# Performance work log

Hardware: AMD Instinct MI355X
Metric: run time of the kernel (lower is better)

The kernel has to match this reference:

```python
import jax, jax.numpy as jnp
import numpy as np

B, L, C, H, DK = 2, 2048, 256, 8, 32  # batch, seq, feaSize, multiNum, dk


def setup_inputs() -> dict:
    key = jax.random.key(0)
    ks = jax.random.split(key, 11)
    w = lambda k, shape: jax.random.normal(k, shape, dtype=jnp.float32) * 0.02
    return {
        'qx': jax.random.normal(ks[0], (B, L, C), dtype=jnp.float32),
        'kx': jax.random.normal(ks[1], (B, L, C), dtype=jnp.float32),
        'vx': jax.random.normal(ks[2], (B, L, C), dtype=jnp.float32),
        'WQ': w(ks[3], (C, H * DK)), 'bQ': w(ks[4], (H * DK,)),
        'WK': w(ks[5], (C, H * DK)), 'bK': w(ks[6], (H * DK,)),
        'WV': w(ks[7], (C, H * DK)), 'bV': w(ks[8], (H * DK,)),
        'WO': w(ks[9], (H * DK, C)), 'bO': w(ks[10], (C,)),
    }


def reference(qx, kx, vx, WQ, bQ, WK, bK, WV, bV, WO, bO):
    b, l, c = qx.shape
    # projections -> (B, H, L, DK)
    q = (qx @ WQ + bQ).reshape(b, l, H, DK).transpose(0, 2, 1, 3)
    k = (kx @ WK + bK).reshape(b, l, H, DK).transpose(0, 2, 1, 3)
    v = (vx @ WV + bV).reshape(b, l, H, DK).transpose(0, 2, 1, 3)

    g = jnp.array([0, l - 1])  # global rows / cols
    scores = jnp.zeros((b, H, l, l), dtype=q.dtype)
    # global rows: q[0], q[L-1] attend to everything
    scores = scores.at[:, :, g, :].set(jnp.einsum('bhgd,bhld->bhgl', q[:, :, g, :], k))
    # global cols: everything attends to k[0], k[L-1]
    scores = scores.at[:, :, :, g].set(jnp.einsum('bhld,bhgd->bhlg', q, k[:, :, g, :]))
    # sliding window: super-diag, sub-diag, main diag (dot products along DK)
    i = jnp.arange(l - 1)
    scores = scores.at[:, :, i, i + 1].set(jnp.sum(q[:, :, :-1] * k[:, :, 1:], axis=-1))
    scores = scores.at[:, :, i + 1, i].set(jnp.sum(q[:, :, 1:] * k[:, :, :-1], axis=-1))
    d = jnp.arange(l)
    scores = scores.at[:, :, d, d].set(jnp.sum(q * k, axis=-1))
    # NOTE: the torch random-block write `scores[:,:,r,:][:,:,:,r] = ...` writes
    # into a copy (chained advanced indexing) and is therefore a no-op; we
    # faithfully omit it. Unfilled positions keep score 0 (not -inf), as in torch.
    scores = scores / np.float32(np.sqrt(DK))
    alpha = jax.nn.softmax(scores, axis=3)
    z = jnp.einsum('bhlm,bhmd->bhld', alpha, v)
    z = z.transpose(0, 2, 1, 3).reshape(b, l, H * DK)
    return z @ WO + bO
```

## Files before the change

### kernel.cpp

```cpp
#include <hip/hip_runtime.h>
#include <hip/hip_bf16.h>

#define B_   2
#define L_   2048
#define C_   256
#define H_   8
#define DK_  32
#define HD_  256
#define RSQRT_DK 0.17677669529663687f

typedef __attribute__((ext_vector_type(8))) short bf16x8;
typedef __attribute__((ext_vector_type(4))) float f32x4;
typedef __attribute__((ext_vector_type(4))) unsigned int u32x4;

__device__ __forceinline__ unsigned short f2bf(float x) {
    unsigned int u = __float_as_uint(x);
    u += 0x7fffu + ((u >> 16) & 1u);
    return (unsigned short)(u >> 16);
}
__device__ __forceinline__ float bf2f(unsigned short h) {
    return __uint_as_float((unsigned int)h << 16);
}

__device__ __forceinline__ uint2 split2(float x0, float x1) {
    __hip_bfloat162 h2 = __float22bfloat162_rn(make_float2(x0, x1));
    unsigned hu; __builtin_memcpy(&hu, &h2, 4);
    const float e0 = __uint_as_float(hu << 16);
    const float e1 = __uint_as_float(hu & 0xffff0000u);
    __hip_bfloat162 l2 = __float22bfloat162_rn(make_float2(x0 - e0, x1 - e1));
    unsigned lu; __builtin_memcpy(&lu, &l2, 4);
    return make_uint2(hu, lu);
}
__device__ __forceinline__ bf16x8 as_bf16x8(u32x4 v) {
    bf16x8 r; __builtin_memcpy(&r, &v, 16); return r;
}

#define WT_IDX(n, k) (((n) << 8) + (((((k) >> 3) ^ ((n) & 7))) << 3) + ((k) & 7))

__device__ __forceinline__ void stage_wT(
    const float* __restrict__ W, int n0, int tid,
    short* __restrict__ WTh, short* __restrict__ WTl)
{
    const int n  = tid & 63;
    const int kc = tid >> 6;
    #pragma unroll
    for (int c8 = 0; c8 < 8; ++c8) {
        const int k0 = kc * 64 + c8 * 8;
        u32x4 hv, lv;
        #pragma unroll
        for (int e = 0; e < 4; ++e) {
            const float x0 = W[(size_t)(k0 + 2 * e)     * HD_ + n0 + n];
            const float x1 = W[(size_t)(k0 + 2 * e + 1) * HD_ + n0 + n];
            const uint2 hl = split2(x0, x1);
            hv[e] = hl.x; lv[e] = hl.y;
        }
        const int o = (n << 8) + ((((k0 >> 3) ^ (n & 7))) << 3);
        *reinterpret_cast<u32x4*>(&WTh[o]) = hv;
        *reinterpret_cast<u32x4*>(&WTl[o]) = lv;
    }
}

__global__ __launch_bounds__(256) void gemm_qkv_fused(
    const float* __restrict__ qx, const float* __restrict__ kx, const float* __restrict__ vx,
    const float* __restrict__ WQ, const float* __restrict__ bQ,
    const float* __restrict__ WK, const float* __restrict__ bK,
    const float* __restrict__ WV, const float* __restrict__ bV,
    float* __restrict__ q, float* __restrict__ k, float* __restrict__ v,
    float* __restrict__ part)
{
    const int bx = blockIdx.x;
    const int yy = blockIdx.y;
    const int proj = yy >> 2, nt = yy & 3;
    const float* A    = proj == 0 ? qx : (proj == 1 ? kx : vx);
    const float* W    = proj == 0 ? WQ : (proj == 1 ? WK : WV);
    const float* bias = proj == 0 ? bQ : (proj == 1 ? bK : bV);
    float* out        = proj == 0 ? q  : (proj == 1 ? k  : v);
    const int n0 = nt * 64;

    __shared__ short WTh[64 * 256];
    __shared__ short WTl[64 * 256];
    __shared__ float red[4][4][16];

    const int tid = threadIdx.x;
    stage_wT(W, n0, tid, WTh, WTl);
    __syncthreads();

    const int w  = tid >> 6;
    const int l  = tid & 63;
    const int lm = l & 15, lk8 = (l >> 4) * 8, cr = (l >> 4) * 4;
    const int R  = bx * 128 + w * 32;

    f32x4 acc[2][4];
    #pragma unroll
    for (int mf = 0; mf < 2; ++mf)
        #pragma unroll
        for (int nf = 0; nf < 4; ++nf)
            acc[mf][nf] = (f32x4){0.f, 0.f, 0.f, 0.f};

    float4 Ab[2][4];
    #define LOAD_A(buf, ks)                                                          \
    {                                                                                \
        const float* p0 = &A[(size_t)(R + lm) * C_ + (ks) * 32 + lk8];               \
        const float* p1 = &A[(size_t)(R + 16 + lm) * C_ + (ks) * 32 + lk8];          \
        Ab[buf][0] = *reinterpret_cast<const float4*>(p0);                           \
        Ab[buf][1] = *reinterpret_cast<const float4*>(p0 + 4);                       \
        Ab[buf][2] = *reinterpret_cast<const float4*>(p1);                           \
        Ab[buf][3] = *reinterpret_cast<const float4*>(p1 + 4);                       \
    }
    LOAD_A(0, 0)
    LOAD_A(1, 1)

    #pragma unroll
    for (int ks = 0; ks < 8; ++ks) {
        const int cur = ks & 1;
        bf16x8 ah[2], al[2];
        #pragma unroll
        for (int mf = 0; mf < 2; ++mf) {
            float4 v0 = Ab[cur][mf * 2], v1 = Ab[cur][mf * 2 + 1];
            u32x4 hq, lq;
            {
                const uint2 r0 = split2(v0.x, v0.y);
                const uint2 r1 = split2(v0.z, v0.w);
                const uint2 r2 = split2(v1.x, v1.y);
                const uint2 r3 = split2(v1.z, v1.w);
                hq[0] = r0.x; lq[0] = r0.y;
                hq[1] = r1.x; lq[1] = r1.y;
                hq[2] = r2.x; lq[2] = r2.y;
                hq[3] = r3.x; lq[3] = r3.y;
            }
            ah[mf] = as_bf16x8(hq);
            al[mf] = as_bf16x8(lq);
        }
        if (ks < 6) LOAD_A(cur, ks + 2)
        bf16x8 Bh[4], Bl[4];
        #pragma unroll
        for (int nf = 0; nf < 4; ++nf) {
            const int o = WT_IDX(nf * 16 + lm, ks * 32 + lk8);
            Bh[nf] = *reinterpret_cast<const bf16x8*>(&WTh[o]);
            Bl[nf] = *reinterpret_cast<const bf16x8*>(&WTl[o]);
        }
        #pragma unroll
        for (int mf = 0; mf < 2; ++mf)
            #pragma unroll
            for (int nf = 0; nf < 4; ++nf) {
                acc[mf][nf] = __builtin_amdgcn_mfma_f32_16x16x32_bf16(ah[mf], Bh[nf], acc[mf][nf], 0, 0, 0);
                acc[mf][nf] = __builtin_amdgcn_mfma_f32_16x16x32_bf16(ah[mf], Bl[nf], acc[mf][nf], 0, 0, 0);
                acc[mf][nf] = __builtin_amdgcn_mfma_f32_16x16x32_bf16(al[mf], Bh[nf], acc[mf][nf], 0, 0, 0);
            }
    }
    #undef LOAD_A

    #pragma unroll
    for (int mf = 0; mf < 2; ++mf)
        #pragma unroll
        for (int nf = 0; nf < 4; ++nf) {
            const int col = n0 + nf * 16 + lm;
            const int h = col >> 5, d = col & 31;
            const float bb = bias[col];
            #pragma unroll
            for (int r = 0; r < 4; ++r) {
                const int m = R + mf * 16 + cr + r;
                const int b = m >> 11, lrow = m & (L_ - 1);
                out[((size_t)(b * H_ + h) * L_ + lrow) * DK_ + d] = acc[mf][nf][r] + bb;
            }
        }

    if (proj == 2) {
        float sl[4];
        #pragma unroll
        for (int nf = 0; nf < 4; ++nf) {
            float s = 0.f;
            #pragma unroll
            for (int mf = 0; mf < 2; ++mf)
                #pragma unroll
                for (int r = 0; r < 4; ++r) s += acc[mf][nf][r];
            s += __shfl_xor(s, 16);
            s += __shfl_xor(s, 32);
            sl[nf] = s;
        }
        if (l < 16) {
            #pragma unroll
            for (int nf = 0; nf < 4; ++nf) red[w][nf][l] = sl[nf];
        }
        __syncthreads();
        if (tid < 64) {
            const int nf = tid >> 4, lmm = tid & 15;
            float tot = red[0][nf][lmm] + red[1][nf][lmm] + red[2][nf][lmm] + red[3][nf][lmm];
            const int col = n0 + nf * 16 + lmm;
            tot += 128.f * bias[col];
            const int h = col >> 5, d = col & 31;
            const int bh = (bx >> 4) * H_ + h;
            part[((size_t)bh * 32 + d) * 16 + (bx & 15)] = tot;
        }
    }
}

#define NSLOT 264
#define VOFF  132

__global__ __launch_bounds__(128) void attn_main(
    const float* __restrict__ q, const float* __restrict__ k,
    const float* __restrict__ v, const float* __restrict__ part,
    float* __restrict__ pm, float* __restrict__ pZ, float* __restrict__ pzv,
    unsigned short* __restrict__ zh, unsigned short* __restrict__ zl)
{
    __shared__ float Sf[NSLOT * 32 + 32];
    float* vs_sh = &Sf[NSLOT * 32];

    #define LDS_F4(slot, u2) (*reinterpret_cast<const float4*>(&Sf[((slot) << 5) + (((u2) ^ ((slot) & 7)) << 2)]))

    const int blk = blockIdx.x;
    const int t = threadIdx.x;

    if (blk < 256) {
        const int bh = blk >> 4, c = blk & 15;
        const int base = c * 128;
        const float* qb = q + (size_t)bh * L_ * DK_;
        const float* kb = k + (size_t)bh * L_ * DK_;
        const float* vb = v + (size_t)bh * L_ * DK_;

        for (int u = t; u < 1056; u += 128) {
            const int slot = u >> 3, quad = u & 7;
            const int row = (slot < 130) ? min(base + slot, L_ - 1)
                                         : ((slot == 130) ? 0 : L_ - 1);
            const size_t go = (size_t)row * DK_ + quad * 4;
            float4 kw = *reinterpret_cast<const float4*>(&kb[go]);
            float4 vw = *reinterpret_cast<const float4*>(&vb[go]);
            const int so = ((quad ^ (slot & 7)) << 2);
            float* dk = &Sf[(slot << 5) + so];
            float* dv = &Sf[((slot + VOFF) << 5) + (((quad ^ ((slot + VOFF) & 7))) << 2)];
            dk[0] = kw.x; dk[1] = kw.y; dk[2] = kw.z; dk[3] = kw.w;
            dv[0] = vw.x; dv[1] = vw.y; dv[2] = vw.z; dv[3] = vw.w;
        }
        if (t < 32) {
            const float4* pp = reinterpret_cast<const float4*>(&part[((size_t)bh * 32 + t) * 16]);
            float4 pa = pp[0], pb = pp[1], pc = pp[2], pd = pp[3];
            vs_sh[t] = pa.x + pa.y + pa.z + pa.w + pb.x + pb.y + pb.z + pb.w
                     + pc.x + pc.y + pc.z + pc.w + pd.x + pd.y + pd.z + pd.w;
        }
        __syncthreads();

        const int i = base + 1 + t;
        if (i <= L_ - 2) {
            float qr[32];
            {
                const float4* qp = reinterpret_cast<const float4*>(&qb[(size_t)i * DK_]);
                #pragma unroll
                for (int u2 = 0; u2 < 8; ++u2) {
                    float4 x = qp[u2];
                    qr[u2 * 4 + 0] = x.x; qr[u2 * 4 + 1] = x.y;
                    qr[u2 * 4 + 2] = x.z; qr[u2 * 4 + 3] = x.w;
                }
            }
            const int ks_[5] = {130, t, t + 1, t + 2, 131};
            float sv[5];
            #pragma unroll
            for (int jj = 0; jj < 5; ++jj) {
                const int s = ks_[jj];
                float p = 0.f;
                #pragma unroll
                for (int u2 = 0; u2 < 8; ++u2) {
                    float4 kv = LDS_F4(s, u2);
                    p += qr[u2 * 4 + 0] * kv.x + qr[u2 * 4 + 1] * kv.y
                       + qr[u2 * 4 + 2] * kv.z + qr[u2 * 4 + 3] * kv.w;
                }
                sv[jj] = p * RSQRT_DK;
            }
            const bool v1 = (i != 1), v3 = (i != L_ - 2);
            float m = fmaxf(0.f, sv[0]);
            m = fmaxf(m, sv[2]); m = fmaxf(m, sv[4]);
            if (v1) m = fmaxf(m, sv[1]);
            if (v3) m = fmaxf(m, sv[3]);
            float e[5];
            e[0] = __expf(sv[0] - m);
            e[1] = v1 ? __expf(sv[1] - m) : 0.f;
            e[2] = __expf(sv[2] - m);
            e[3] = v3 ? __expf(sv[3] - m) : 0.f;
            e[4] = __expf(sv[4] - m);
            const int ns = 3 + (int)v1 + (int)v3;
            const float e0 = __expf(-m);
            const float Z = e[0] + e[1] + e[2] + e[3] + e[4] + (float)(L_ - ns) * e0;
            const float rZ = 1.f / Z;
            const float f1 = v1 ? 1.f : 0.f, f3 = v3 ? 1.f : 0.f;

            u32x4 zhq[4], zlq[4];
            #pragma unroll
            for (int u2 = 0; u2 < 8; ++u2) {
                float4 x0 = LDS_F4(VOFF + 130,   u2);
                float4 x1 = LDS_F4(VOFF + t,     u2);
                float4 x2 = LDS_F4(VOFF + t + 1, u2);
                float4 x3 = LDS_F4(VOFF + t + 2, u2);
                float4 x4 = LDS_F4(VOFF + 131,   u2);
                float a0[4] = {x0.x, x0.y, x0.z, x0.w};
                float a1[4] = {x1.x, x1.y, x1.z, x1.w};
                float a2[4] = {x2.x, x2.y, x2.z, x2.w};
                float a3[4] = {x3.x, x3.y, x3.z, x3.w};
                float a4[4] = {x4.x, x4.y, x4.z, x4.w};
                float zd4[4];
                #pragma unroll
                for (int e2 = 0; e2 < 4; ++e2) {
                    const int d = u2 * 4 + e2;
                    const float num = e[0] * a0[e2] + e[1] * a1[e2] + e[2] * a2[e2]
                                    + e[3] * a3[e2] + e[4] * a4[e2];
                    const float vp = a0[e2] + f1 * a1[e2] + a2[e2] + f3 * a3[e2] + a4[e2];
                    zd4[e2] = (num + e0 * (vs_sh[d] - vp)) * rZ;
                }
                const uint2 p0 = split2(zd4[0], zd4[1]);
                const uint2 p1 = split2(zd4[2], zd4[3]);
                zhq[u2 >> 1][(u2 & 1) * 2 + 0] = p0.x;
                zhq[u2 >> 1][(u2 & 1) * 2 + 1] = p1.x;
                zlq[u2 >> 1][(u2 & 1) * 2 + 0] = p0.y;
                zlq[u2 >> 1][(u2 & 1) * 2 + 1] = p1.y;
            }
            const int b = bh >> 3, h = bh & 7;
            const size_t o = (size_t)(b * L_ + i) * HD_ + h * DK_;
            #pragma unroll
            for (int u4 = 0; u4 < 4; ++u4) {
                *reinterpret_cast<u32x4*>(&zh[o + u4 * 8]) = zhq[u4];
                *reinterpret_cast<u32x4*>(&zl[o + u4 * 8]) = zlq[u4];
            }
        }
    } else {
        const int blk2 = blk - 256;
        const int bh = blk2 >> 5;
        const int pair = (blk2 >> 4) & 1;
        const int chunk = blk2 & 15;
        const int r = pair ? (L_ - 1) : 0;
        const int j0 = chunk * 128;
        const float* qb = q + (size_t)bh * L_ * DK_;
        const float* kb = k + (size_t)bh * L_ * DK_;
        const float* vb = v + (size_t)bh * L_ * DK_;

        float* qs  = Sf;
        float* sc  = Sf + 32;
        float* red = Sf + 160;
        float* pzs = Sf + 192;

        if (t < 32) qs[t] = qb[(size_t)r * DK_ + t];
        __syncthreads();

        const int j = j0 + t;
        const float4* kr = reinterpret_cast<const float4*>(&kb[(size_t)j * DK_]);
        float p = 0.f;
        #pragma unroll
        for (int u = 0; u < 8; ++u) {
            float4 kv = kr[u];
            p += qs[u * 4 + 0] * kv.x + qs[u * 4 + 1] * kv.y
               + qs[u * 4 + 2] * kv.z + qs[u * 4 + 3] * kv.w;
        }
        p *= RSQRT_DK;

        float lm = p;
        #pragma unroll
        for (int off = 32; off; off >>= 1) lm = fmaxf(lm, __shfl_xor(lm, off, 64));
        if ((t & 63) == 0) red[t >> 6] = lm;
        __syncthreads();
        const float m = fmaxf(red[0], red[1]);

        const float e = __expf(p - m);
        sc[t] = e;
        float ls = e;
        #pragma unroll
        for (int off = 32; off; off >>= 1) ls += __shfl_xor(ls, off, 64);
        if ((t & 63) == 0) red[2 + (t >> 6)] = ls;
        __syncthreads();
        const float Zc = red[2] + red[3];

        const int d = t & 31, g = t >> 5;
        float acc = 0.f;
        #pragma unroll 4
        for (int jj = 0; jj < 32; ++jj)
            acc += sc[g * 32 + jj] * vb[(size_t)(j0 + g * 32 + jj) * DK_ + d];
        pzs[g * 32 + d] = acc;
        __syncthreads();
        if (g == 0) {
            const float s2 = pzs[d] + pzs[32 + d] + pzs[64 + d] + pzs[96 + d];
            pzv[(size_t)blk2 * 32 + d] = s2;
        }
        if (t == 0) { pm[blk2] = m; pZ[blk2] = Zc; }
    }
    #undef LDS_F4
}

__global__ __launch_bounds__(256) void gemm_out_fused(
    const unsigned short* __restrict__ zh_c, unsigned short* __restrict__ zh,
    unsigned short* __restrict__ zl,
    const float* __restrict__ pm, const float* __restrict__ pZ,
    const float* __restrict__ pzv,
    const float* __restrict__ WO, const float* __restrict__ bO,
    float* __restrict__ out)
{
    const int bx = blockIdx.x;
    const int nt = blockIdx.y;
    const int n0 = nt * 64;

    __shared__ short WTh[64 * 256];
    __shared__ short WTl[64 * 256];

    const int tid = threadIdx.x;
    stage_wT(WO, n0, tid, WTh, WTl);

    int zrow = -1;
    if      (bx == 0)  zrow = 0;
    else if (bx == 31) zrow = L_ - 1;
    else if (bx == 32) zrow = L_;
    else if (bx == 63) zrow = 2 * L_ - 1;
    if (zrow >= 0) {
        const int h = tid >> 5, d = tid & 31;
        const int b = zrow >> 11;
        const int r = zrow & (L_ - 1);
        const int pair = r ? 1 : 0;
        const int rowIdx = (b * H_ + h) * 2 + pair;
        const int base = rowIdx * 16;
        float m = -1e30f;
        #pragma unroll
        for (int c = 0; c < 16; ++c) m = fmaxf(m, pm[base + c]);
        float Z = 0.f, zd = 0.f;
        #pragma unroll
        for (int c = 0; c < 16; ++c) {
            const float w2 = __expf(pm[base + c] - m);
            Z  += pZ[base + c] * w2;
            zd += pzv[(size_t)(base + c) * 32 + d] * w2;
        }
        zd /= Z;
        const size_t o = (size_t)zrow * HD_ + h * DK_ + d;
        const unsigned short hb = f2bf(zd);
        zh[o] = hb;
        zl[o] = f2bf(zd - bf2f(hb));
    }
    __syncthreads();

    const int w  = tid >> 6;
    const int l  = tid & 63;
    const int lm = l & 15, lk8 = (l >> 4) * 8, cr = (l >> 4) * 4;
    const int R  = bx * 64 + w * 16;

    f32x4 acc[4];
    #pragma unroll
    for (int nf = 0; nf < 4; ++nf) acc[nf] = (f32x4){0.f, 0.f, 0.f, 0.f};

    bf16x8 Ah[2], Al[2];
    #define LOAD_Z(buf, ks)                                                          \
    {                                                                                \
        const size_t o = (size_t)(R + lm) * HD_ + (ks) * 32 + lk8;                   \
        Ah[buf] = *reinterpret_cast<const bf16x8*>(&zh_c[o]);                        \
        Al[buf] = *reinterpret_cast<const bf16x8*>(&zl[o]);                          \
    }
    LOAD_Z(0, 0)
    LOAD_Z(1, 1)

    #pragma unroll
    for (int ks = 0; ks < 8; ++ks) {
        const int cur = ks & 1;
        const bf16x8 a_h = Ah[cur], a_l = Al[cur];
        if (ks < 6) LOAD_Z(cur, ks + 2)
        #pragma unroll
        for (int nf = 0; nf < 4; ++nf) {
            const int o = WT_IDX(nf * 16 + lm, ks * 32 + lk8);
            const bf16x8 b_h = *reinterpret_cast<const bf16x8*>(&WTh[o]);
            const bf16x8 b_l = *reinterpret_cast<const bf16x8*>(&WTl[o]);
            acc[nf] = __builtin_amdgcn_mfma_f32_16x16x32_bf16(a_h, b_h, acc[nf], 0, 0, 0);
            acc[nf] = __builtin_amdgcn_mfma_f32_16x16x32_bf16(a_h, b_l, acc[nf], 0, 0, 0);
            acc[nf] = __builtin_amdgcn_mfma_f32_16x16x32_bf16(a_l, b_h, acc[nf], 0, 0, 0);
        }
    }
    #undef LOAD_Z

    #pragma unroll
    for (int nf = 0; nf < 4; ++nf) {
        const int col = n0 + nf * 16 + lm;
        const float bb = bO[col];
        #pragma unroll
        for (int r = 0; r < 4; ++r) {
            const int m = R + cr + r;
            out[(size_t)m * HD_ + col] = acc[nf][r] + bb;
        }
    }
}

extern "C" void kernel_launch(void* const* d_in, const int* in_sizes, int n_in,
                              void* d_out, int out_size, void* d_ws, size_t ws_size,
                              hipStream_t stream)
{
    const float* qx = (const float*)d_in[0];
    const float* kx = (const float*)d_in[1];
    const float* vx = (const float*)d_in[2];
    const float* WQ = (const float*)d_in[3];
    const float* bQ = (const float*)d_in[4];
    const float* WK = (const float*)d_in[5];
    const float* bK = (const float*)d_in[6];
    const float* WV = (const float*)d_in[7];
    const float* bV = (const float*)d_in[8];
    const float* WO = (const float*)d_in[9];
    const float* bO = (const float*)d_in[10];
    float* out = (float*)d_out;

    char* wsb = (char*)d_ws;
    float*          q    = (float*)(wsb);
    float*          k    = (float*)(wsb + (4u  << 20));
    float*          v    = (float*)(wsb + (8u  << 20));
    unsigned short* zh   = (unsigned short*)(wsb + (12u << 20));
    unsigned short* zl   = (unsigned short*)(wsb + (14u << 20));
    float*          part = (float*)(wsb + (16u << 20));
    float*          pm   = (float*)(wsb + (16u << 20) + (1u << 16));
    float*          pZ   = pm + 512;
    float*          pzv  = pm + 1024;

    gemm_qkv_fused<<<dim3(32, 12), 256, 0, stream>>>(qx, kx, vx, WQ, bQ, WK, bK, WV, bV, q, k, v, part);
    attn_main<<<768, 128, 0, stream>>>(q, k, v, part, pm, pZ, pzv, zh, zl);
    gemm_out_fused<<<dim3(64, 4), 256, 0, stream>>>(zh, zh, zl, pm, pZ, pzv, WO, bO, out);
}
```

Measured before the change: 35.16 us.

## Pre-split WO once in QKV kernel and read K/V from global in attention

An extra row of blocks in the QKV projection kernel converts WO into transposed bf16 hi/lo arrays in workspace. The output GEMM then copies those arrays straight into shared memory instead of re-splitting WO in every block. The attention kernel drops its LDS staging of K/V windows and reads the five needed K/V rows per query directly from global memory through cache. This cuts LDS footprint and a sync-bound staging loop, at the cost of more scattered global loads and an extra workspace buffer.

```diff
diff --git a/kernel.cpp b/kernel.cpp
--- a/kernel.cpp
+++ b/kernel.cpp
@@ -60,16 +60,50 @@
     }
 }
 
+__device__ __forceinline__ void stage_wT_copy(
+    const unsigned short* __restrict__ wTp, int n0, int tid,
+    short* __restrict__ WTh, short* __restrict__ WTl)
+{
+    #pragma unroll
+    for (int it = 0; it < 8; ++it) {
+        const int c = tid + it * 256;
+        const int n = c >> 5, k8 = c & 31;
+        const size_t go = (size_t)(n0 + n) * 256 + k8 * 8;
+        const int o = (n << 8) + ((k8 ^ (n & 7)) << 3);
+        *reinterpret_cast<bf16x8*>(&WTh[o]) = *reinterpret_cast<const bf16x8*>(&wTp[go]);
+        *reinterpret_cast<bf16x8*>(&WTl[o]) = *reinterpret_cast<const bf16x8*>(&wTp[65536 + go]);
+    }
+}
+
 __global__ __launch_bounds__(256) void gemm_qkv_fused(
     const float* __restrict__ qx, const float* __restrict__ kx, const float* __restrict__ vx,
     const float* __restrict__ WQ, const float* __restrict__ bQ,
     const float* __restrict__ WK, const float* __restrict__ bK,
     const float* __restrict__ WV, const float* __restrict__ bV,
+    const float* __restrict__ WO, unsigned short* __restrict__ wT,
     float* __restrict__ q, float* __restrict__ k, float* __restrict__ v,
     float* __restrict__ part)
 {
     const int bx = blockIdx.x;
     const int yy = blockIdx.y;
+    const int tid = threadIdx.x;
+
+    if (yy == 12) {
+        const int n  = bx * 8 + (tid >> 5);
+        const int k8 = (tid & 31) * 8;
+        u32x4 hv, lv;
+        #pragma unroll
+        for (int e = 0; e < 4; ++e) {
+            const float x0 = WO[(size_t)(k8 + 2 * e)     * HD_ + n];
+            const float x1 = WO[(size_t)(k8 + 2 * e + 1) * HD_ + n];
+            const uint2 hl = split2(x0, x1);
+            hv[e] = hl.x; lv[e] = hl.y;
+        }
+        *reinterpret_cast<u32x4*>(&wT[(size_t)n * 256 + k8])         = hv;
+        *reinterpret_cast<u32x4*>(&wT[65536 + (size_t)n * 256 + k8]) = lv;
+        return;
+    }
+
     const int proj = yy >> 2, nt = yy & 3;
     const float* A    = proj == 0 ? qx : (proj == 1 ? kx : vx);
     const float* W    = proj == 0 ? WQ : (proj == 1 ? WK : WV);
@@ -81,7 +115,6 @@
     __shared__ short WTl[64 * 256];
     __shared__ float red[4][4][16];
 
-    const int tid = threadIdx.x;
     stage_wT(W, n0, tid, WTh, WTl);
     __syncthreads();
 
@@ -195,19 +228,13 @@
     }
 }
 
-#define NSLOT 264
-#define VOFF  132
-
 __global__ __launch_bounds__(128) void attn_main(
     const float* __restrict__ q, const float* __restrict__ k,
     const float* __restrict__ v, const float* __restrict__ part,
     float* __restrict__ pm, float* __restrict__ pZ, float* __restrict__ pzv,
     unsigned short* __restrict__ zh, unsigned short* __restrict__ zl)
 {
-    __shared__ float Sf[NSLOT * 32 + 32];
-    float* vs_sh = &Sf[NSLOT * 32];
-
-    #define LDS_F4(slot, u2) (*reinterpret_cast<const float4*>(&Sf[((slot) << 5) + (((u2) ^ ((slot) & 7)) << 2)]))
+    __shared__ float Sf[324];
 
     const int blk = blockIdx.x;
     const int t = threadIdx.x;
@@ -218,20 +245,8 @@
         const float* qb = q + (size_t)bh * L_ * DK_;
         const float* kb = k + (size_t)bh * L_ * DK_;
         const float* vb = v + (size_t)bh * L_ * DK_;
-
-        for (int u = t; u < 1056; u += 128) {
-            const int slot = u >> 3, quad = u & 7;
-            const int row = (slot < 130) ? min(base + slot, L_ - 1)
-                                         : ((slot == 130) ? 0 : L_ - 1);
-            const size_t go = (size_t)row * DK_ + quad * 4;
-            float4 kw = *reinterpret_cast<const float4*>(&kb[go]);
-            float4 vw = *reinterpret_cast<const float4*>(&vb[go]);
-            const int so = ((quad ^ (slot & 7)) << 2);
-            float* dk = &Sf[(slot << 5) + so];
-            float* dv = &Sf[((slot + VOFF) << 5) + (((quad ^ ((slot + VOFF) & 7))) << 2)];
-            dk[0] = kw.x; dk[1] = kw.y; dk[2] = kw.z; dk[3] = kw.w;
-            dv[0] = vw.x; dv[1] = vw.y; dv[2] = vw.z; dv[3] = vw.w;
-        }
+        float* vs_sh = Sf;
+
         if (t < 32) {
             const float4* pp = reinterpret_cast<const float4*>(&part[((size_t)bh * 32 + t) * 16]);
             float4 pa = pp[0], pb = pp[1], pc = pp[2], pd = pp[3];
@@ -252,15 +267,15 @@
                     qr[u2 * 4 + 2] = x.z; qr[u2 * 4 + 3] = x.w;
                 }
             }
-            const int ks_[5] = {130, t, t + 1, t + 2, 131};
+            const int rows[5] = {0, i - 1, i, i + 1, L_ - 1};
             float sv[5];
             #pragma unroll
             for (int jj = 0; jj < 5; ++jj) {
-                const int s = ks_[jj];
+                const float4* kp = reinterpret_cast<const float4*>(&kb[(size_t)rows[jj] * DK_]);
                 float p = 0.f;
                 #pragma unroll
                 for (int u2 = 0; u2 < 8; ++u2) {
-                    float4 kv = LDS_F4(s, u2);
+                    float4 kv = kp[u2];
                     p += qr[u2 * 4 + 0] * kv.x + qr[u2 * 4 + 1] * kv.y
                        + qr[u2 * 4 + 2] * kv.z + qr[u2 * 4 + 3] * kv.w;
                 }
@@ -283,14 +298,16 @@
             const float rZ = 1.f / Z;
             const float f1 = v1 ? 1.f : 0.f, f3 = v3 ? 1.f : 0.f;
 
+            const float4* vp0 = reinterpret_cast<const float4*>(&vb[0]);
+            const float4* vp1 = reinterpret_cast<const float4*>(&vb[(size_t)rows[1] * DK_]);
+            const float4* vp2 = reinterpret_cast<const float4*>(&vb[(size_t)i * DK_]);
+            const float4* vp3 = reinterpret_cast<const float4*>(&vb[(size_t)rows[3] * DK_]);
+            const float4* vp4 = reinterpret_cast<const float4*>(&vb[(size_t)(L_ - 1) * DK_]);
+
             u32x4 zhq[4], zlq[4];
             #pragma unroll
             for (int u2 = 0; u2 < 8; ++u2) {
-                float4 x0 = LDS_F4(VOFF + 130,   u2);
-                float4 x1 = LDS_F4(VOFF + t,     u2);
-                float4 x2 = LDS_F4(VOFF + t + 1, u2);
-                float4 x3 = LDS_F4(VOFF + t + 2, u2);
-                float4 x4 = LDS_F4(VOFF + 131,   u2);
+                float4 x0 = vp0[u2], x1 = vp1[u2], x2 = vp2[u2], x3 = vp3[u2], x4 = vp4[u2];
                 float a0[4] = {x0.x, x0.y, x0.z, x0.w};
                 float a1[4] = {x1.x, x1.y, x1.z, x1.w};
                 float a2[4] = {x2.x, x2.y, x2.z, x2.w};
@@ -302,8 +319,8 @@
                     const int d = u2 * 4 + e2;
                     const float num = e[0] * a0[e2] + e[1] * a1[e2] + e[2] * a2[e2]
                                     + e[3] * a3[e2] + e[4] * a4[e2];
-                    const float vp = a0[e2] + f1 * a1[e2] + a2[e2] + f3 * a3[e2] + a4[e2];
-                    zd4[e2] = (num + e0 * (vs_sh[d] - vp)) * rZ;
+                    const float vp_ = a0[e2] + f1 * a1[e2] + a2[e2] + f3 * a3[e2] + a4[e2];
+                    zd4[e2] = (num + e0 * (vs_sh[d] - vp_)) * rZ;
                 }
                 const uint2 p0 = split2(zd4[0], zd4[1]);
                 const uint2 p1 = split2(zd4[2], zd4[3]);
@@ -379,7 +396,6 @@
         }
         if (t == 0) { pm[blk2] = m; pZ[blk2] = Zc; }
     }
-    #undef LDS_F4
 }
 
 __global__ __launch_bounds__(256) void gemm_out_fused(
@@ -387,7 +403,7 @@
     unsigned short* __restrict__ zl,
     const float* __restrict__ pm, const float* __restrict__ pZ,
     const float* __restrict__ pzv,
-    const float* __restrict__ WO, const float* __restrict__ bO,
+    const unsigned short* __restrict__ wT, const float* __restrict__ bO,
     float* __restrict__ out)
 {
     const int bx = blockIdx.x;
@@ -398,7 +414,7 @@
     __shared__ short WTl[64 * 256];
 
     const int tid = threadIdx.x;
-    stage_wT(WO, n0, tid, WTh, WTl);
+    stage_wT_copy(wT, n0, tid, WTh, WTl);
 
     int zrow = -1;
     if      (bx == 0)  zrow = 0;
@@ -505,8 +521,9 @@
     float*          pm   = (float*)(wsb + (16u << 20) + (1u << 16));
     float*          pZ   = pm + 512;
     float*          pzv  = pm + 1024;
-
-    gemm_qkv_fused<<<dim3(32, 12), 256, 0, stream>>>(qx, kx, vx, WQ, bQ, WK, bK, WV, bV, q, k, v, part);
+    unsigned short* wT   = (unsigned short*)(wsb + (17u << 20));
+
+    gemm_qkv_fused<<<dim3(32, 13), 256, 0, stream>>>(qx, kx, vx, WQ, bQ, WK, bK, WV, bV, WO, wT, q, k, v, part);
     attn_main<<<768, 128, 0, stream>>>(q, k, v, part, pm, pZ, pzv, zh, zl);
-    gemm_out_fused<<<dim3(64, 4), 256, 0, stream>>>(zh, zh, zl, pm, pZ, pzv, WO, bO, out);
-}
+    gemm_out_fused<<<dim3(64, 4), 256, 0, stream>>>(zh, zh, zl, pm, pZ, pzv, wT, bO, out);
+}
```

New measurement: 33.85 us. 3.7% less time.
